# Kernel tuning notes

Measured on AMD Instinct MI355X. Metric: run time of the kernel, lower is better.

Reference implementation:

```python
import jax, jax.numpy as jnp
import numpy as np

KY, KX = 3, 3  # kernel_size from init_kwargs


def setup_inputs() -> dict:
    key = jax.random.key(0)
    x = jax.random.normal(key, (8, 64, 256, 256), dtype=jnp.float32)
    return {"x": x}


def reference(x):
    # NMS: mask = x > max over 3x3 replicate-padded neighborhood EXCLUDING center.
    # Note: the torch conv kernel zeroes the center row, so the center output
    # channel is all zeros and the max implicitly includes 0 — we replicate that
    # by initializing the running max to zeros.
    ky, kx = KY, KX
    py, px = (ky - 1) // 2, (kx - 1) // 2
    H, W = x.shape[-2], x.shape[-1]
    xp = jnp.pad(x, ((0, 0), (0, 0), (py, py), (px, px)), mode='edge')  # replicate pad
    numel = ky * kx
    center = numel // 2
    max_non_center = jnp.zeros_like(x)  # zeroed-center channel participates in max
    for i in range(numel):  # fixed small kernel window, unrolled (8 shifts)
        if i == center:
            continue
        dy, dx = divmod(i, kx)
        max_non_center = jnp.maximum(max_non_center, xp[..., dy:dy + H, dx:dx + W])
    mask = x > max_non_center
    return x * mask.astype(x.dtype)
```

## Files before the change

### kernel.cpp

```cpp
#include <hip/hip_runtime.h>


#define NMS_H 256
#define NMS_W 256
#define PLANE (NMS_H * NMS_W)

typedef float f4_t __attribute__((ext_vector_type(4)));

struct HV {
    float4 h;
    float4 lr;
};

__device__ __forceinline__ HV rowmax(const float4 v, const int tx) {
    float l = __shfl_up(v.w, 1, 64);
    float r = __shfl_down(v.x, 1, 64);
    if (tx == 0)  l = v.x;
    if (tx == 63) r = v.w;
    HV o;
    o.h.x = fmaxf(l,   fmaxf(v.x, v.y));
    o.h.y = fmaxf(v.x, fmaxf(v.y, v.z));
    o.h.z = fmaxf(v.y, fmaxf(v.z, v.w));
    o.h.w = fmaxf(v.z, fmaxf(v.w, r));
    o.lr.x = fmaxf(l,   v.y);
    o.lr.y = fmaxf(v.x, v.z);
    o.lr.z = fmaxf(v.y, v.w);
    o.lr.w = fmaxf(v.z, r);
    return o;
}

__global__ __launch_bounds__(256) void nms2d_kernel(const float* __restrict__ x,
                                                    float* __restrict__ out) {
    const int blk     = blockIdx.x;
    const int logical = (blk >> 3) + (blk & 7) * (32768 / 8);

    const int plane_idx = logical >> 6;
    const int rg        = logical & 63;
    const int tx        = threadIdx.x & 63;
    const int r         = rg * 4 + (threadIdx.x >> 6);
    const int col4      = tx * 4;

    const float* pl = x + (size_t)plane_idx * PLANE;

    const int rm = max(r - 1, 0);
    const int rp = min(r + 1, NMS_H - 1);
    const float4 va = *reinterpret_cast<const float4*>(pl + rm * NMS_W + col4);
    const float4 vc = *reinterpret_cast<const float4*>(pl + r  * NMS_W + col4);
    const float4 vb = *reinterpret_cast<const float4*>(pl + rp * NMS_W + col4);

    const HV ma = rowmax(va, tx);
    const HV mc = rowmax(vc, tx);
    const HV mb = rowmax(vb, tx);

    f4_t o;
    float m;
    m = fmaxf(0.0f, fmaxf(fmaxf(ma.h.x, mb.h.x), mc.lr.x)); o.x = (vc.x > m) ? vc.x : 0.0f;
    m = fmaxf(0.0f, fmaxf(fmaxf(ma.h.y, mb.h.y), mc.lr.y)); o.y = (vc.y > m) ? vc.y : 0.0f;
    m = fmaxf(0.0f, fmaxf(fmaxf(ma.h.z, mb.h.z), mc.lr.z)); o.z = (vc.z > m) ? vc.z : 0.0f;
    m = fmaxf(0.0f, fmaxf(fmaxf(ma.h.w, mb.h.w), mc.lr.w)); o.w = (vc.w > m) ? vc.w : 0.0f;

    *reinterpret_cast<f4_t*>(out + (size_t)plane_idx * PLANE + r * NMS_W + col4) = o;
}

extern "C" void kernel_launch(void* const* d_in, const int* in_sizes, int n_in,
                              void* d_out, int out_size, void* d_ws, size_t ws_size,
                              hipStream_t stream) {
    const float* x = (const float*)d_in[0];
    float* out = (float*)d_out;

    dim3 block(256);
    dim3 grid(32768);
    nms2d_kernel<<<grid, block, 0, stream>>>(x, out);
}
```

Baseline: 226.6 us.

## Process four rows per thread to reuse vertical neighbor loads

New measurement: 229.7 us. No clear change (+1.4%).

```diff
diff --git a/kernel.cpp b/kernel.cpp
--- a/kernel.cpp
+++ b/kernel.cpp
@@ -4,6 +4,7 @@
 #define NMS_H 256
 #define NMS_W 256
 #define PLANE (NMS_H * NMS_W)
+#define GRID_BLOCKS 8192
 
 typedef float f4_t __attribute__((ext_vector_type(4)));
 
@@ -29,37 +30,51 @@
     return o;
 }
 
-__global__ __launch_bounds__(256) void nms2d_kernel(const float* __restrict__ x,
-                                                    float* __restrict__ out) {
+__device__ __forceinline__ f4_t nmspick(const float4 vc, const float4 ha,
+                                        const float4 hb, const float4 lrc) {
+    f4_t o;
+    float m;
+    m = fmaxf(0.0f, fmaxf(fmaxf(ha.x, hb.x), lrc.x)); o.x = (vc.x > m) ? vc.x : 0.0f;
+    m = fmaxf(0.0f, fmaxf(fmaxf(ha.y, hb.y), lrc.y)); o.y = (vc.y > m) ? vc.y : 0.0f;
+    m = fmaxf(0.0f, fmaxf(fmaxf(ha.z, hb.z), lrc.z)); o.z = (vc.z > m) ? vc.z : 0.0f;
+    m = fmaxf(0.0f, fmaxf(fmaxf(ha.w, hb.w), lrc.w)); o.w = (vc.w > m) ? vc.w : 0.0f;
+    return o;
+}
+
+__global__ __launch_bounds__(256, 4) void nms2d_kernel(const float* __restrict__ x,
+                                                       float* __restrict__ out) {
     const int blk     = blockIdx.x;
-    const int logical = (blk >> 3) + (blk & 7) * (32768 / 8);
+    const int logical = (blk >> 3) + (blk & 7) * (GRID_BLOCKS / 8);
 
-    const int plane_idx = logical >> 6;
-    const int rg        = logical & 63;
+    const int plane_idx = logical >> 4;
+    const int rg        = logical & 15;
     const int tx        = threadIdx.x & 63;
-    const int r         = rg * 4 + (threadIdx.x >> 6);
+    const int R         = rg * 16 + (threadIdx.x >> 6) * 4;
     const int col4      = tx * 4;
 
-    const float* pl = x + (size_t)plane_idx * PLANE;
+    const float* pl = x + (size_t)plane_idx * PLANE + col4;
 
-    const int rm = max(r - 1, 0);
-    const int rp = min(r + 1, NMS_H - 1);
-    const float4 va = *reinterpret_cast<const float4*>(pl + rm * NMS_W + col4);
-    const float4 vc = *reinterpret_cast<const float4*>(pl + r  * NMS_W + col4);
-    const float4 vb = *reinterpret_cast<const float4*>(pl + rp * NMS_W + col4);
+    const int rm = max(R - 1, 0);
+    const int rp = min(R + 4, NMS_H - 1);
+    const float4 vm = *reinterpret_cast<const float4*>(pl + rm      * NMS_W);
+    const float4 v0 = *reinterpret_cast<const float4*>(pl + (R + 0) * NMS_W);
+    const float4 v1 = *reinterpret_cast<const float4*>(pl + (R + 1) * NMS_W);
+    const float4 v2 = *reinterpret_cast<const float4*>(pl + (R + 2) * NMS_W);
+    const float4 v3 = *reinterpret_cast<const float4*>(pl + (R + 3) * NMS_W);
+    const float4 vp = *reinterpret_cast<const float4*>(pl + rp      * NMS_W);
 
-    const HV ma = rowmax(va, tx);
-    const HV mc = rowmax(vc, tx);
-    const HV mb = rowmax(vb, tx);
+    const HV hm = rowmax(vm, tx);
+    const HV h0 = rowmax(v0, tx);
+    const HV h1 = rowmax(v1, tx);
+    const HV h2 = rowmax(v2, tx);
+    const HV h3 = rowmax(v3, tx);
+    const HV hp = rowmax(vp, tx);
 
-    f4_t o;
-    float m;
-    m = fmaxf(0.0f, fmaxf(fmaxf(ma.h.x, mb.h.x), mc.lr.x)); o.x = (vc.x > m) ? vc.x : 0.0f;
-    m = fmaxf(0.0f, fmaxf(fmaxf(ma.h.y, mb.h.y), mc.lr.y)); o.y = (vc.y > m) ? vc.y : 0.0f;
-    m = fmaxf(0.0f, fmaxf(fmaxf(ma.h.z, mb.h.z), mc.lr.z)); o.z = (vc.z > m) ? vc.z : 0.0f;
-    m = fmaxf(0.0f, fmaxf(fmaxf(ma.h.w, mb.h.w), mc.lr.w)); o.w = (vc.w > m) ? vc.w : 0.0f;
-
-    *reinterpret_cast<f4_t*>(out + (size_t)plane_idx * PLANE + r * NMS_W + col4) = o;
+    float* po = out + (size_t)plane_idx * PLANE + col4;
+    *reinterpret_cast<f4_t*>(po + (R + 0) * NMS_W) = nmspick(v0, hm.h, h1.h, h0.lr);
+    *reinterpret_cast<f4_t*>(po + (R + 1) * NMS_W) = nmspick(v1, h0.h, h2.h, h1.lr);
+    *reinterpret_cast<f4_t*>(po + (R + 2) * NMS_W) = nmspick(v2, h1.h, h3.h, h2.lr);
+    *reinterpret_cast<f4_t*>(po + (R + 3) * NMS_W) = nmspick(v3, h2.h, hp.h, h3.lr);
 }
 
 extern "C" void kernel_launch(void* const* d_in, const int* in_sizes, int n_in,
@@ -69,6 +84,6 @@
     float* out = (float*)d_out;
 
     dim3 block(256);
-    dim3 grid(32768);
+    dim3 grid(GRID_BLOCKS);
     nms2d_kernel<<<grid, block, 0, stream>>>(x, out);
 }
```
